# Optimization experiments

Hardware: AMD Instinct MI355X
Metric: run time of the kernel (lower is better)

The kernel has to match this reference:

```python
import math
import jax, jax.numpy as jnp
import numpy as np

B, T, D = 8, 2048, 256
N_TICKS, DT, P_MIN, P_MAX = 3, 1.0, 2.0, 4.0


def setup_inputs() -> dict:
    key = jax.random.key(0)
    ks = jax.random.split(key, 16)
    s = 1.0 / math.sqrt(D)
    w = lambda k: jax.random.normal(k, (D, D), jnp.float32) * s
    zb = jnp.zeros((D,), jnp.float32)
    return {
        "z": jax.random.normal(ks[0], (B, T, D), jnp.float32),
        "in_w": w(ks[1]), "in_b": zb,
        "ln_g": jnp.ones((D,), jnp.float32), "ln_b": zb,
        "q_w": w(ks[2]), "q_b": zb,
        "k_w": w(ks[3]), "k_b": zb,
        "v_w": w(ks[4]), "v_b": zb,
        "o_w": w(ks[5]), "o_b": zb,
        "log_tau": jnp.zeros((D,), jnp.float32),
        "p1_w": w(ks[6]), "p1_b": zb,
        "p2_w": w(ks[7]), "p2_b": zb,
    }


def _layernorm(x, g, b, eps=1e-5):
    mu = jnp.mean(x, axis=-1, keepdims=True)
    var = jnp.var(x, axis=-1, keepdims=True)
    return (x - mu) * jax.lax.rsqrt(var + eps) * g + b


def _lin(x, w, b):
    return x @ w.T + b


def reference(z, in_w, in_b, ln_g, ln_b, q_w, q_b, k_w, k_b, v_w, v_b,
              o_w, o_b, log_tau, p1_w, p1_b, p2_w, p2_b):
    tau = jnp.exp(log_tau)  # [d]
    inv_sqrt_d = 1.0 / math.sqrt(D)
    uniform = 1.0 / T
    pred_losses, eff_ps = [], []
    for _ in range(N_TICKS):
        h = _layernorm(_lin(z, in_w, in_b), ln_g, ln_b)
        Q, K, V = _lin(h, q_w, q_b), _lin(h, k_w, k_b), _lin(h, v_w, v_b)
        sim = jnp.einsum('btd,bsd->bts', Q, K) * inv_sqrt_d  # [B,T,T]
        attn = jax.nn.softmax(sim, axis=-1)
        row_max = jnp.max(attn, axis=-1)  # [B,T]
        conf = (jnp.mean(row_max, axis=-1) - uniform) / (1.0 - uniform + 1e-6)
        conf = jnp.clip(conf, 0.0, 1.0)  # [B]
        eff_p = P_MIN + (P_MAX - P_MIN) * conf
        eff_ps.append(jax.lax.stop_gradient(eff_p))
        attn_sharp = jax.nn.softmax(sim * eff_p[:, None, None], axis=-1)
        context = jnp.einsum('bts,bsd->btd', attn_sharp, V)
        target = _lin(context, o_w, o_b)
        z_pred = _lin(jax.nn.relu(_lin(z, p1_w, p1_b)), p2_w, p2_b)
        dz = (target - z) / (tau + 1e-6)
        z_next = z + DT * dz
        pred_losses.append(jnp.mean((z_pred - jax.lax.stop_gradient(z_next)) ** 2))
        z = z_next
    pred_loss_mean = jnp.mean(jnp.stack(pred_losses))
    eff_p_mean = jnp.mean(jnp.concatenate(eff_ps))
    return z, pred_loss_mean, eff_p_mean
```

## Files before the change

kernel.cpp:

```cpp
#include <hip/hip_runtime.h>
#include <math.h>

#define Bn 8
#define Tn 2048
#define Dn 256
#define NTICK 3
#define NROWS (Bn*Tn)
#define ABM 64
#define NBLKA (NROWS/ABM)
#define BS 64
#define GM 64
#define NBLKG (NROWS/GM)
#define WP 65536

typedef unsigned int u32;
typedef unsigned short u16;
typedef __attribute__((ext_vector_type(8))) short bf16x8;
typedef __attribute__((ext_vector_type(4))) float f32x4;

__device__ __forceinline__ float bf2f(u32 u){
  union { u32 i; float f; } x; x.i = u << 16; return x.f;
}
__device__ __forceinline__ u16 f2bf(float f){
  union { float f; u32 i; } x; x.f = f;
  u32 r = (x.i + 0x7fffu + ((x.i >> 16) & 1u)) >> 16;
  return (u16)r;
}
__device__ __forceinline__ void gld_lds16(const u16* gsrc, u16* ldst){
  __builtin_amdgcn_global_load_lds(
      (const __attribute__((address_space(1))) u32*)(const void*)gsrc,
      (__attribute__((address_space(3))) u32*)(void*)ldst, 16, 0, 0);
}

__device__ __forceinline__ void stage_A(const u16* __restrict__ A, int row0, char* smem){
  const int tid = threadIdx.x, lane = tid & 63, w = tid >> 6;
  #pragma unroll
  for (int r=0;r<8;++r){
    int s = w*16 + 2*r + (lane>>5);
    int slot = (lane & 31) ^ (s & 7);
    gld_lds16(A + (size_t)(row0 + s)*Dn + slot*8, (u16*)(smem + (w*16 + 2*r)*512));
  }
}
__device__ __forceinline__ void load_frags(const char* smem, bf16x8* af){
  const int tid = threadIdx.x, lane = tid & 63, w = tid >> 6;
  const int l7 = lane & 7, g = (lane >> 4) & 3, q15 = lane & 15;
  const char* ab = smem + (w*16 + q15)*512;
  #pragma unroll
  for (int kk=0;kk<8;++kk) af[kk] = *(const bf16x8*)(ab + 16*((4*kk+g)^l7));
}
__device__ __forceinline__ void stage_Wchunk(const u16* __restrict__ W, int c, char* wbuf){
  const int tid = threadIdx.x, lane = tid & 63, w = tid >> 6;
  #pragma unroll
  for (int r=0;r<2;++r){
    int rl = w*4 + 2*r + (lane>>5);
    int slot = (lane & 31) ^ (rl & 7);
    gld_lds16(W + (size_t)(c*16 + rl)*Dn + slot*8, (u16*)(wbuf + (w*4 + 2*r)*512));
  }
}
__device__ __forceinline__ void load_wfrags(const char* wbuf, bf16x8* wf){
  const int lane = threadIdx.x & 63;
  const int l7 = lane & 7, g = (lane >> 4) & 3, q15 = lane & 15;
  const char* wb_ = wbuf + q15*512;
  #pragma unroll
  for (int kk=0;kk<8;++kk) wf[kk] = *(const bf16x8*)(wb_ + 16*((4*kk+g)^l7));
}
__device__ __forceinline__ void zero_acc(f32x4* acc){
  #pragma unroll
  for (int nt=0;nt<16;++nt) acc[nt] = (f32x4){0.f,0.f,0.f,0.f};
}
#define CHUNK_STEP(c, NC, PLANE_OF, IDX_OF)                                    \
  asm volatile("s_waitcnt lgkmcnt(0)" ::: "memory");                           \
  if ((c) < (NC)-2) { asm volatile("s_waitcnt vmcnt(2)" ::: "memory"); }       \
  else              { asm volatile("s_waitcnt vmcnt(0)" ::: "memory"); }       \
  __builtin_amdgcn_sched_barrier(0);                                           \
  __builtin_amdgcn_s_barrier();                                                \
  if ((c)+3 < (NC)) stage_Wchunk(PLANE_OF((c)+3), IDX_OF((c)+3), ring + (((c)+3)&3)*8192);

__global__ void k_prep(const float* __restrict__ s0, const float* __restrict__ s1,
                       const float* __restrict__ s2, const float* __restrict__ s3,
                       const float* __restrict__ s4, const float* __restrict__ s5,
                       const float* __restrict__ s6, u16* __restrict__ dst){
  int y = blockIdx.y;
  const float* s = (y==0)?s0:(y==1)?s1:(y==2)?s2:(y==3)?s3:(y==4)?s4:(y==5)?s5:s6;
  int i = (blockIdx.x*256 + threadIdx.x)*4;
  float4 v = *(const float4*)(s + i);
  u16 h0=f2bf(v.x), h1=f2bf(v.y), h2=f2bf(v.z), h3=f2bf(v.w);
  uint2 hi, lo;
  hi.x = (u32)h0 | ((u32)h1 << 16);
  hi.y = (u32)h2 | ((u32)h3 << 16);
  lo.x = (u32)f2bf(v.x - bf2f(h0)) | ((u32)f2bf(v.y - bf2f(h1)) << 16);
  lo.y = (u32)f2bf(v.z - bf2f(h2)) | ((u32)f2bf(v.w - bf2f(h3)) << 16);
  *(uint2*)(dst + (size_t)y*WP + i) = hi;
  *(uint2*)(dst + (size_t)(7+y)*WP + i) = lo;
}

__global__ void k_split(const float* __restrict__ s, u16* __restrict__ dh, u16* __restrict__ dl,
                        float* __restrict__ stats){
  if (blockIdx.x == 0 && threadIdx.x < 64) stats[threadIdx.x] = 0.f;
  int i = (blockIdx.x*256 + threadIdx.x)*4;
  float4 v = *(const float4*)(s + i);
  u16 h0=f2bf(v.x), h1=f2bf(v.y), h2=f2bf(v.z), h3=f2bf(v.w);
  uint2 hi, lo;
  hi.x = (u32)h0 | ((u32)h1 << 16);
  hi.y = (u32)h2 | ((u32)h3 << 16);
  lo.x = (u32)f2bf(v.x - bf2f(h0)) | ((u32)f2bf(v.y - bf2f(h1)) << 16);
  lo.y = (u32)f2bf(v.z - bf2f(h2)) | ((u32)f2bf(v.w - bf2f(h3)) << 16);
  *(uint2*)(dh + i) = hi;
  *(uint2*)(dl + i) = lo;
}

__global__ __launch_bounds__(256) void k_gemm_ln(
    const u16* __restrict__ Ahi, const u16* __restrict__ Alo,
    const u16* __restrict__ Whi, const u16* __restrict__ Wlo,
    const float* __restrict__ bias, const float* __restrict__ gamma, const float* __restrict__ beta,
    u16* __restrict__ h)
{
  __shared__ __align__(16) char smem[65536];
  char* ring = smem;
  f32x4 acc[16];
  const int row0 = blockIdx.x * GM;
  stage_A(Ahi, row0, smem);
  stage_A(Alo, row0, smem + 32768);
  asm volatile("s_waitcnt vmcnt(0)" ::: "memory");
  __builtin_amdgcn_sched_barrier(0);
  bf16x8 afh[8], afl[8];
  load_frags(smem, afh);
  load_frags(smem + 32768, afl);
  asm volatile("s_waitcnt lgkmcnt(0)" ::: "memory");
  __builtin_amdgcn_sched_barrier(0);
  __builtin_amdgcn_s_barrier();
  zero_acc(acc);
  #define LN_PL(i) ((i) < 16 ? Whi : Wlo)
  #define LN_IX(i) ((i) & 15)
  stage_Wchunk(LN_PL(0), LN_IX(0), ring + 0*8192);
  stage_Wchunk(LN_PL(1), LN_IX(1), ring + 1*8192);
  stage_Wchunk(LN_PL(2), LN_IX(2), ring + 2*8192);
  asm volatile("s_waitcnt vmcnt(4)" ::: "memory");
  __builtin_amdgcn_sched_barrier(0);
  __builtin_amdgcn_s_barrier();
  for (int c=0; c<32; ++c){
    bf16x8 wf[8];
    load_wfrags(ring + (c&3)*8192, wf);
    int nt = c & 15;
    if (c < 16){
      #pragma unroll
      for (int kk=0;kk<8;++kk)
        acc[nt] = __builtin_amdgcn_mfma_f32_16x16x32_bf16(afh[kk], wf[kk], acc[nt], 0,0,0);
      #pragma unroll
      for (int kk=0;kk<8;++kk)
        acc[nt] = __builtin_amdgcn_mfma_f32_16x16x32_bf16(afl[kk], wf[kk], acc[nt], 0,0,0);
    } else {
      #pragma unroll
      for (int kk=0;kk<8;++kk)
        acc[nt] = __builtin_amdgcn_mfma_f32_16x16x32_bf16(afh[kk], wf[kk], acc[nt], 0,0,0);
    }
    CHUNK_STEP(c, 32, LN_PL, LN_IX)
  }
  const int tid = threadIdx.x, lane = tid & 63, w = tid >> 6;
  const int g4 = lane >> 4, q15 = lane & 15;
  float bcol[16], gcol[16], becol[16];
  #pragma unroll
  for (int nt=0;nt<16;++nt){
    int col = nt*16 + q15;
    bcol[nt] = bias[col]; gcol[nt] = gamma[col]; becol[nt] = beta[col];
  }
  float mu[4], rstd[4];
  #pragma unroll
  for (int j=0;j<4;++j){
    float s=0.f, q=0.f;
    #pragma unroll
    for (int nt=0;nt<16;++nt){ float v = acc[nt][j] + bcol[nt]; s += v; q += v*v; }
    #pragma unroll
    for (int off=1; off<16; off<<=1){ s += __shfl_xor(s,off); q += __shfl_xor(q,off); }
    float m = s*(1.f/Dn);
    mu[j] = m; rstd[j] = rsqrtf(q*(1.f/Dn) - m*m + 1e-5f);
  }
  const size_t rbase = (size_t)(row0 + w*16 + g4*4);
  #pragma unroll
  for (int nt=0;nt<16;++nt){
    #pragma unroll
    for (int j=0;j<4;++j){
      float v = (acc[nt][j] + bcol[nt] - mu[j])*rstd[j]*gcol[nt] + becol[nt];
      h[(rbase+j)*Dn + nt*16 + q15] = f2bf(v);
    }
  }
}

__global__ __launch_bounds__(256) void k_gemm_qkv(
    const u16* __restrict__ h, const u16* __restrict__ wbf,
    const float* __restrict__ qb, const float* __restrict__ kb, const float* __restrict__ vb,
    u16* __restrict__ Qo, u16* __restrict__ Ko, u16* __restrict__ Vo)
{
  const u16 *Whi, *Wlo; const float* bias; u16* out;
  if (blockIdx.y == 0){ Whi = wbf + 1*WP; Wlo = wbf + 8*WP;  bias = qb; out = Qo; }
  else if (blockIdx.y == 1){ Whi = wbf + 2*WP; Wlo = wbf + 9*WP;  bias = kb; out = Ko; }
  else { Whi = wbf + 3*WP; Wlo = wbf + 10*WP; bias = vb; out = Vo; }
  __shared__ __align__(16) char smem[65536];
  char* ring = smem + 32768;
  f32x4 acc[16];
  const int row0 = blockIdx.x * GM;
  stage_A(h, row0, smem);
  #define QK_PL(i) ((i) < 16 ? Whi : Wlo)
  #define QK_IX(i) ((i) & 15)
  stage_Wchunk(QK_PL(0), QK_IX(0), ring + 0*8192);
  stage_Wchunk(QK_PL(1), QK_IX(1), ring + 1*8192);
  stage_Wchunk(QK_PL(2), QK_IX(2), ring + 2*8192);
  asm volatile("s_waitcnt vmcnt(4)" ::: "memory");
  __builtin_amdgcn_sched_barrier(0);
  bf16x8 af[8];
  load_frags(smem, af);
  zero_acc(acc);
  __builtin_amdgcn_s_barrier();
  for (int c=0; c<32; ++c){
    bf16x8 wf[8];
    load_wfrags(ring + (c&3)*8192, wf);
    int nt = c & 15;
    #pragma unroll
    for (int kk=0;kk<8;++kk)
      acc[nt] = __builtin_amdgcn_mfma_f32_16x16x32_bf16(af[kk], wf[kk], acc[nt], 0,0,0);
    CHUNK_STEP(c, 32, QK_PL, QK_IX)
  }
  const int tid = threadIdx.x, lane = tid & 63, w = tid >> 6;
  const int g4 = lane >> 4, q15 = lane & 15;
  const size_t rbase = (size_t)(row0 + w*16 + g4*4);
  #pragma unroll
  for (int nt=0;nt<16;++nt){
    float bc = bias[nt*16 + q15];
    #pragma unroll
    for (int j=0;j<4;++j)
      out[(rbase+j)*Dn + nt*16 + q15] = f2bf(acc[nt][j] + bc);
  }
}

__global__ __launch_bounds__(256) void k_gemm_update(
    const u16* __restrict__ Chi, const u16* __restrict__ Clo,
    const u16* __restrict__ Whi, const u16* __restrict__ Wlo,
    const float* __restrict__ ob,
    const u16* __restrict__ zhi_old, const u16* __restrict__ zlo_old,
    const float* __restrict__ log_tau,
    u16* __restrict__ zhi_new, u16* __restrict__ zlo_new,
    float* __restrict__ zout)
{
  __shared__ __align__(16) char smem[65536];
  char* ring = smem;
  f32x4 acc[16];
  const int row0 = blockIdx.x * GM;
  stage_A(Chi, row0, smem);
  stage_A(Clo, row0, smem + 32768);
  asm volatile("s_waitcnt vmcnt(0)" ::: "memory");
  __builtin_amdgcn_sched_barrier(0);
  bf16x8 afh[8], afl[8];
  load_frags(smem, afh);
  load_frags(smem + 32768, afl);
  asm volatile("s_waitcnt lgkmcnt(0)" ::: "memory");
  __builtin_amdgcn_sched_barrier(0);
  __builtin_amdgcn_s_barrier();
  zero_acc(acc);
  stage_Wchunk(LN_PL(0), LN_IX(0), ring + 0*8192);
  stage_Wchunk(LN_PL(1), LN_IX(1), ring + 1*8192);
  stage_Wchunk(LN_PL(2), LN_IX(2), ring + 2*8192);
  asm volatile("s_waitcnt vmcnt(4)" ::: "memory");
  __builtin_amdgcn_sched_barrier(0);
  __builtin_amdgcn_s_barrier();
  for (int c=0; c<32; ++c){
    bf16x8 wf[8];
    load_wfrags(ring + (c&3)*8192, wf);
    int nt = c & 15;
    if (c < 16){
      #pragma unroll
      for (int kk=0;kk<8;++kk)
        acc[nt] = __builtin_amdgcn_mfma_f32_16x16x32_bf16(afh[kk], wf[kk], acc[nt], 0,0,0);
      #pragma unroll
      for (int kk=0;kk<8;++kk)
        acc[nt] = __builtin_amdgcn_mfma_f32_16x16x32_bf16(afl[kk], wf[kk], acc[nt], 0,0,0);
    } else {
      #pragma unroll
      for (int kk=0;kk<8;++kk)
        acc[nt] = __builtin_amdgcn_mfma_f32_16x16x32_bf16(afh[kk], wf[kk], acc[nt], 0,0,0);
    }
    CHUNK_STEP(c, 32, LN_PL, LN_IX)
  }
  const int tid = threadIdx.x, lane = tid & 63, w = tid >> 6;
  const int g4 = lane >> 4, q15 = lane & 15;
  const size_t rbase = (size_t)(row0 + w*16 + g4*4);
  #pragma unroll
  for (int nt=0;nt<16;++nt){
    int col = nt*16 + q15;
    float bc = ob[col];
    float invt = 1.f/(expf(log_tau[col]) + 1e-6f);
    #pragma unroll
    for (int j=0;j<4;++j){
      size_t idx = (rbase+j)*Dn + col;
      float zo = bf2f(zhi_old[idx]) + bf2f(zlo_old[idx]);
      float zn = zo + (acc[nt][j] + bc - zo)*invt;
      u16 zh = f2bf(zn);
      zhi_new[idx] = zh;
      zlo_new[idx] = f2bf(zn - bf2f(zh));
      if (zout) zout[idx] = zn;
    }
  }
}

__global__ __launch_bounds__(256) void k_gemm_relu(
    const u16* __restrict__ A, const u16* __restrict__ Wb, const float* __restrict__ bias,
    u16* __restrict__ t1)
{
  __shared__ __align__(16) char smem[65536];
  char* ring = smem + 32768;
  f32x4 acc[16];
  const int row0 = blockIdx.x * GM;
  stage_A(A, row0, smem);
  #define W1_PL(i) (Wb)
  #define W1_IX(i) (i)
  stage_Wchunk(Wb, 0, ring + 0*8192);
  stage_Wchunk(Wb, 1, ring + 1*8192);
  stage_Wchunk(Wb, 2, ring + 2*8192);
  asm volatile("s_waitcnt vmcnt(4)" ::: "memory");
  __builtin_amdgcn_sched_barrier(0);
  bf16x8 af[8];
  load_frags(smem, af);
  zero_acc(acc);
  __builtin_amdgcn_s_barrier();
  for (int c=0; c<16; ++c){
    bf16x8 wf[8];
    load_wfrags(ring + (c&3)*8192, wf);
    #pragma unroll
    for (int kk=0;kk<8;++kk)
      acc[c] = __builtin_amdgcn_mfma_f32_16x16x32_bf16(af[kk], wf[kk], acc[c], 0,0,0);
    CHUNK_STEP(c, 16, W1_PL, W1_IX)
  }
  const int tid = threadIdx.x, lane = tid & 63, w = tid >> 6;
  const int g4 = lane >> 4, q15 = lane & 15;
  const size_t rbase = (size_t)(row0 + w*16 + g4*4);
  #pragma unroll
  for (int nt=0;nt<16;++nt){
    float bc = bias[nt*16 + q15];
    #pragma unroll
    for (int j=0;j<4;++j)
      t1[(rbase+j)*Dn + nt*16 + q15] = f2bf(fmaxf(acc[nt][j] + bc, 0.f));
  }
}

__global__ __launch_bounds__(256) void k_gemm_loss(
    const u16* __restrict__ t1, const u16* __restrict__ Wb, const float* __restrict__ bias,
    const u16* __restrict__ zhi_new, const u16* __restrict__ zlo_new,
    float* __restrict__ loss_acc)
{
  __shared__ __align__(16) char smem[65536];
  __shared__ float red[4];
  char* ring = smem + 32768;
  f32x4 acc[16];
  const int row0 = blockIdx.x * GM;
  stage_A(t1, row0, smem);
  stage_Wchunk(Wb, 0, ring + 0*8192);
  stage_Wchunk(Wb, 1, ring + 1*8192);
  stage_Wchunk(Wb, 2, ring + 2*8192);
  asm volatile("s_waitcnt vmcnt(4)" ::: "memory");
  __builtin_amdgcn_sched_barrier(0);
  bf16x8 af[8];
  load_frags(smem, af);
  zero_acc(acc);
  __builtin_amdgcn_s_barrier();
  for (int c=0; c<16; ++c){
    bf16x8 wf[8];
    load_wfrags(ring + (c&3)*8192, wf);
    #pragma unroll
    for (int kk=0;kk<8;++kk)
      acc[c] = __builtin_amdgcn_mfma_f32_16x16x32_bf16(af[kk], wf[kk], acc[c], 0,0,0);
    CHUNK_STEP(c, 16, W1_PL, W1_IX)
  }
  const int tid = threadIdx.x, lane = tid & 63, w = tid >> 6;
  const int g4 = lane >> 4, q15 = lane & 15;
  const size_t rbase = (size_t)(row0 + w*16 + g4*4);
  float lsum = 0.f;
  #pragma unroll
  for (int nt=0;nt<16;++nt){
    float bc = bias[nt*16 + q15];
    #pragma unroll
    for (int j=0;j<4;++j){
      size_t idx = (rbase+j)*Dn + nt*16 + q15;
      float zn = bf2f(zhi_new[idx]) + bf2f(zlo_new[idx]);
      float dn = acc[nt][j] + bc - zn;
      lsum += dn*dn;
    }
  }
  #pragma unroll
  for (int off=1; off<64; off<<=1) lsum += __shfl_xor(lsum, off);
  if (lane == 0) red[w] = lsum;
  __syncthreads();
  if (tid == 0) atomicAdd(loss_acc, red[0]+red[1]+red[2]+red[3]);
}

__global__ __launch_bounds__(256) void k_passA(
    const u16* __restrict__ Qg, const u16* __restrict__ Kg,
    float* __restrict__ conf_b)
{
  __shared__ __align__(16) char smem[65536];
  const int tid = threadIdx.x;
  const int lane = tid & 63, w = tid >> 6;
  const int l7 = lane & 7, g = (lane >> 4) & 3, q15 = lane & 15;
  const int row0 = blockIdx.x * ABM;
  const int b = row0 >> 11;
  const size_t kbase = (size_t)b * Tn * Dn;

  #pragma unroll
  for (int r=0;r<8;++r){
    int s = w*16 + 2*r + (lane>>5);
    int slot = (lane & 31) ^ (s & 7);
    gld_lds16(Qg + (size_t)(row0 + s)*Dn + slot*8, (u16*)(smem + (w*16 + 2*r)*512));
  }
  asm volatile("s_waitcnt vmcnt(0)" ::: "memory");
  __builtin_amdgcn_sched_barrier(0);
  bf16x8 qf[8];
  {
    const char* qb = smem + (w*16 + q15)*512;
    #pragma unroll
    for (int kk=0;kk<8;++kk) qf[kk] = *(const bf16x8*)(qb + 16*((4*kk+g)^l7));
  }
  asm volatile("s_waitcnt lgkmcnt(0)" ::: "memory");
  __builtin_amdgcn_sched_barrier(0);
  #pragma unroll
  for (int r=0;r<8;++r){
    int s = w*16 + 2*r + (lane>>5);
    int slot = (lane & 31) ^ (s & 7);
    gld_lds16(Kg + kbase + (size_t)(s)*Dn + slot*8, (u16*)(smem + 32768 + (w*16 + 2*r)*512));
  }
  #pragma unroll
  for (int r=0;r<8;++r){
    int s = w*16 + 2*r + (lane>>5);
    int slot = (lane & 31) ^ (s & 7);
    gld_lds16(Kg + kbase + (size_t)(BS + s)*Dn + slot*8, (u16*)(smem + (w*16 + 2*r)*512));
  }
  asm volatile("s_waitcnt vmcnt(8)" ::: "memory");
  __builtin_amdgcn_sched_barrier(0);
  __builtin_amdgcn_s_barrier();

  float m_run = -INFINITY, l_run = 0.f;
  int cur = 1;
  for (int tile=0; tile<Tn/BS; ++tile){
    const char* kb = smem + cur*32768;
    f32x4 sc[4];
    #pragma unroll
    for (int ms=0;ms<4;++ms) sc[ms] = (f32x4){0.f,0.f,0.f,0.f};
    #pragma unroll
    for (int kk=0;kk<8;++kk){
      #pragma unroll
      for (int ms=0;ms<4;++ms){
        bf16x8 kf = *(const bf16x8*)(kb + (ms*16+q15)*512 + 16*((4*kk+g)^l7));
        sc[ms] = __builtin_amdgcn_mfma_f32_16x16x32_bf16(kf, qf[kk], sc[ms], 0,0,0);
      }
    }
    float vmax = -INFINITY;
    float vals[16];
    #pragma unroll
    for (int ms=0;ms<4;++ms){
      #pragma unroll
      for (int j=0;j<4;++j){ float v = sc[ms][j]*0.0625f; vals[ms*4+j]=v; vmax=fmaxf(vmax,v); }
    }
    vmax = fmaxf(vmax, __shfl_xor(vmax,16));
    vmax = fmaxf(vmax, __shfl_xor(vmax,32));
    float mnew = fmaxf(m_run, vmax);
    float corr = __expf(m_run - mnew);
    float esum = 0.f;
    #pragma unroll
    for (int t2=0;t2<16;++t2) esum += __expf(vals[t2]-mnew);
    esum += __shfl_xor(esum,16); esum += __shfl_xor(esum,32);
    l_run = l_run*corr + esum;
    m_run = mnew;

    asm volatile("s_waitcnt vmcnt(0)" ::: "memory");
    __builtin_amdgcn_sched_barrier(0);
    __builtin_amdgcn_s_barrier();
    if (tile < Tn/BS - 2){
      #pragma unroll
      for (int r=0;r<8;++r){
        int s = w*16 + 2*r + (lane>>5);
        int slot = (lane & 31) ^ (s & 7);
        gld_lds16(Kg + kbase + (size_t)((tile+2)*BS + s)*Dn + slot*8,
                  (u16*)(smem + cur*32768 + (w*16 + 2*r)*512));
      }
    }
    cur ^= 1;
  }
  float r1 = 1.f/l_run;
  #pragma unroll
  for (int off=1; off<64; off<<=1) r1 += __shfl_xor(r1, off);
  if (lane==0) atomicAdd(conf_b + b, r1*0.25f);
}

#define KB0 0
#define KB1 32768
#define VT0 65536
#define VT1 98304
#define PST 131072
__global__ __launch_bounds__(512) void k_passB(
    const u16* __restrict__ Qg, const u16* __restrict__ Kg, const u16* __restrict__ Vg,
    const float* __restrict__ conf_sum, u16* __restrict__ Chi, u16* __restrict__ Clo)
{
  __shared__ __align__(16) char smem[139264];
  const int tid = threadIdx.x;
  const int lane = tid & 63, w = tid >> 6;
  const int qg = w & 3, hs = w >> 2;
  const int l7 = lane & 7, g = (lane >> 4) & 3, q15 = lane & 15;
  const int row0 = blockIdx.x * ABM;
  const int b = row0 >> 11;
  const size_t kbase = (size_t)b * Tn * Dn;
  float mean_rm = conf_sum[b] * (1.f/Tn);
  float uniform = 1.f/Tn;
  float conf = fminf(fmaxf((mean_rm - uniform)/(1.f - uniform + 1e-6f), 0.f), 1.f);
  const float scale = (2.f + 2.f*conf) * 0.0625f;
  const int tid2 = tid & 255;
  const int dblk = tid2 >> 3, sblk = tid2 & 7;
  uint4 vreg[8];
  const int NT = Tn/BS;

  if (hs == 0){
    #pragma unroll
    for (int r=0;r<8;++r){
      int s = w*16 + 2*r + (lane>>5);
      int slot = (lane & 31) ^ (s & 7);
      gld_lds16(Qg + (size_t)(row0 + s)*Dn + slot*8, (u16*)(smem + KB0 + (w*16 + 2*r)*512));
    }
  } else {
    const u16* vsrc = Vg + kbase + (size_t)(sblk*8)*Dn + dblk*8;
    #pragma unroll
    for (int si=0; si<8; ++si) vreg[si] = *(const uint4*)(vsrc + (size_t)si*Dn);
  }
  __syncthreads();
  bf16x8 qf[8];
  {
    const char* qb = smem + KB0 + (qg*16 + q15)*512;
    #pragma unroll
    for (int kk=0;kk<8;++kk) qf[kk] = *(const bf16x8*)(qb + 16*((4*kk+g)^l7));
  }
  __syncthreads();
  if (hs == 0){
    #pragma unroll
    for (int r=0;r<8;++r){
      int s = w*16 + 2*r + (lane>>5);
      int slot = (lane & 31) ^ (s & 7);
      gld_lds16(Kg + kbase + (size_t)(s)*Dn + slot*8, (u16*)(smem + KB0 + (w*16 + 2*r)*512));
    }
    #pragma unroll
    for (int r=0;r<8;++r){
      int s = w*16 + 2*r + (lane>>5);
      int slot = (lane & 31) ^ (s & 7);
      gld_lds16(Kg + kbase + (size_t)(BS + s)*Dn + slot*8, (u16*)(smem + KB1 + (w*16 + 2*r)*512));
    }
    asm volatile("s_waitcnt vmcnt(8)" ::: "memory");
    __builtin_amdgcn_sched_barrier(0);
  } else {
    const u32* rw = (const u32*)vreg;
    #pragma unroll
    for (int dl=0; dl<8; ++dl){
      int wi = dl >> 1;
      u32 sel = (dl & 1) ? 0x07060302u : 0x05040100u;
      uint4 o;
      o.x = __builtin_amdgcn_perm(rw[1*4+wi], rw[0*4+wi], sel);
      o.y = __builtin_amdgcn_perm(rw[3*4+wi], rw[2*4+wi], sel);
      o.z = __builtin_amdgcn_perm(rw[5*4+wi], rw[4*4+wi], sel);
      o.w = __builtin_amdgcn_perm(rw[7*4+wi], rw[6*4+wi], sel);
      int d = dblk*8 + dl;
      *(uint4*)(smem + VT0 + d*128 + 16*(sblk ^ dl)) = o;
    }
    asm volatile("s_waitcnt lgkmcnt(0)" ::: "memory");
    __builtin_amdgcn_sched_barrier(0);
  }
  __builtin_amdgcn_s_barrier();

  float m_run = -INFINITY, l_run = 0.f;
  f32x4 oa[16];
  #pragma unroll
  for (int md=0;md<16;++md) oa[md] = (f32x4){0.f,0.f,0.f,0.f};

  char* pbase = smem + PST + w*1024 + q15*64;
  const int psw = q15 & 3;

  int cur = 0;
  for (int tile=0; tile<NT; ++tile){
    const char* kbuf = smem + (cur ? KB1 : KB0);
    const char* vbuf = smem + (cur ? VT1 : VT0);
    char* vbuf_n = (char*)smem + (cur ? VT0 : VT1);
    if (hs == 1 && tile < NT-1){
      const u16* vsrc = Vg + kbase + (size_t)((tile+1)*BS + sblk*8)*Dn + dblk*8;
      #pragma unroll
      for (int si=0; si<8; ++si) vreg[si] = *(const uint4*)(vsrc + (size_t)si*Dn);
    }
    f32x4 sc[2];
    sc[0] = (f32x4){0.f,0.f,0.f,0.f};
    sc[1] = (f32x4){0.f,0.f,0.f,0.f};
    #pragma unroll
    for (int kk=0;kk<8;++kk){
      #pragma unroll
      for (int msl=0;msl<2;++msl){
        int msg = 2*hs + msl;
        bf16x8 kf = *(const bf16x8*)(kbuf + (msg*16+q15)*512 + 16*((4*kk+g)^l7));
        sc[msl] = __builtin_amdgcn_mfma_f32_16x16x32_bf16(kf, qf[kk], sc[msl], 0,0,0);
      }
    }
    float vmax = -INFINITY;
    float vals[8];
    #pragma unroll
    for (int msl=0;msl<2;++msl){
      #pragma unroll
      for (int j=0;j<4;++j){ float v = sc[msl][j]*scale; vals[msl*4+j]=v; vmax=fmaxf(vmax,v); }
    }
    vmax = fmaxf(vmax, __shfl_xor(vmax,16));
    vmax = fmaxf(vmax, __shfl_xor(vmax,32));
    float mnew = fmaxf(m_run, vmax);
    float corr = __expf(m_run - mnew);
    float esum = 0.f;
    #pragma unroll
    for (int t2=0;t2<8;++t2){ float p = __expf(vals[t2]-mnew); vals[t2]=p; esum += p; }
    esum += __shfl_xor(esum,16); esum += __shfl_xor(esum,32);
    l_run = l_run*corr + esum;
    m_run = mnew;
    #pragma unroll
    for (int md=0;md<16;++md) oa[md] *= corr;
    #pragma unroll
    for (int msl=0;msl<2;++msl){
      uint2 pw;
      pw.x = (u32)f2bf(vals[msl*4+0]) | ((u32)f2bf(vals[msl*4+1]) << 16);
      pw.y = (u32)f2bf(vals[msl*4+2]) | ((u32)f2bf(vals[msl*4+3]) << 16);
      int slot = (2*msl + (g>>1)) ^ psw;
      *(uint2*)(pbase + slot*16 + (g&1)*8) = pw;
    }
    asm volatile("s_waitcnt lgkmcnt(0)" ::: "memory");
    __builtin_amdgcn_sched_barrier(0);
    {
      bf16x8 pf = *(const bf16x8*)(pbase + ((g ^ psw)*16));
      #pragma unroll
      for (int md=0; md<16; ++md){
        bf16x8 vf = *(const bf16x8*)(vbuf + (md*16+q15)*128 + 16*((4*hs+g)^l7));
        oa[md] = __builtin_amdgcn_mfma_f32_16x16x32_bf16(vf, pf, oa[md], 0,0,0);
      }
    }
    if (hs == 1){
      if (tile < NT-1){
        asm volatile("s_waitcnt vmcnt(0)" ::: "memory");
        __builtin_amdgcn_sched_barrier(0);
        const u32* rw = (const u32*)vreg;
        #pragma unroll
        for (int dl=0; dl<8; ++dl){
          int wi = dl >> 1;
          u32 sel = (dl & 1) ? 0x07060302u : 0x05040100u;
          uint4 o;
          o.x = __builtin_amdgcn_perm(rw[1*4+wi], rw[0*4+wi], sel);
          o.y = __builtin_amdgcn_perm(rw[3*4+wi], rw[2*4+wi], sel);
          o.z = __builtin_amdgcn_perm(rw[5*4+wi], rw[4*4+wi], sel);
          o.w = __builtin_amdgcn_perm(rw[7*4+wi], rw[6*4+wi], sel);
          int d = dblk*8 + dl;
          *(uint4*)(vbuf_n + d*128 + 16*(sblk ^ dl)) = o;
        }
      }
      asm volatile("s_waitcnt lgkmcnt(0)" ::: "memory");
    } else {
      asm volatile("s_waitcnt vmcnt(0) lgkmcnt(0)" ::: "memory");
    }
    __builtin_amdgcn_sched_barrier(0);
    __builtin_amdgcn_s_barrier();
    if (hs == 0 && tile < NT-2){
      #pragma unroll
      for (int r=0;r<8;++r){
        int s = w*16 + 2*r + (lane>>5);
        int slot = (lane & 31) ^ (s & 7);
        gld_lds16(Kg + kbase + (size_t)((tile+2)*BS + s)*Dn + slot*8,
                  (u16*)(smem + (cur ? KB1 : KB0) + (w*16 + 2*r)*512));
      }
    }
    cur ^= 1;
  }
  __syncthreads();
  if (hs == 1){
    char* ob_ = smem + (qg*64 + lane)*256;
    #pragma unroll
    for (int md=0; md<16; ++md)
      *(f32x4*)(ob_ + (md ^ q15)*16) = oa[md];
    float2 ml; ml.x = m_run; ml.y = l_run;
    *(float2*)(smem + VT0 + (qg*64 + lane)*8) = ml;
  }
  __syncthreads();
  if (hs == 0){
    float2 ml = *(const float2*)(smem + VT0 + (qg*64 + lane)*8);
    float m = fmaxf(m_run, ml.x);
    float ca = __expf(m_run - m), cb = __expf(ml.x - m);
    float l = l_run*ca + ml.y*cb;
    float inv = 1.f / l;
    const char* ob_ = smem + (qg*64 + lane)*256;
    const size_t rr = (size_t)(row0 + qg*16 + q15)*Dn + g*4;
    #pragma unroll
    for (int md=0; md<16; ++md){
      f32x4 ob = *(const f32x4*)(ob_ + (md ^ q15)*16);
      float v0 = (oa[md][0]*ca + ob[0]*cb)*inv;
      float v1 = (oa[md][1]*ca + ob[1]*cb)*inv;
      float v2 = (oa[md][2]*ca + ob[2]*cb)*inv;
      float v3 = (oa[md][3]*ca + ob[3]*cb)*inv;
      uint2 hi, lo;
      u16 h0=f2bf(v0), h1=f2bf(v1), h2=f2bf(v2), h3=f2bf(v3);
      hi.x = (u32)h0 | ((u32)h1 << 16);
      hi.y = (u32)h2 | ((u32)h3 << 16);
      lo.x = (u32)f2bf(v0 - bf2f(h0)) | ((u32)f2bf(v1 - bf2f(h1)) << 16);
      lo.y = (u32)f2bf(v2 - bf2f(h2)) | ((u32)f2bf(v3 - bf2f(h3)) << 16);
      *(uint2*)(Chi + rr + md*16) = hi;
      *(uint2*)(Clo + rr + md*16) = lo;
    }
  }
}

__global__ void k_finalize(const float* __restrict__ loss3, const float* __restrict__ conf_sum,
                           float* __restrict__ out_scalars){
  if (threadIdx.x == 0){
    float ls = (loss3[0]+loss3[1]+loss3[2]) * (1.f/(3.f*NROWS*Dn));
    float es = 0.f;
    float uniform = 1.f/Tn;
    #pragma unroll
    for (int i=0;i<NTICK*Bn;++i){
      float mean_rm = conf_sum[i] * (1.f/Tn);
      float conf = fminf(fmaxf((mean_rm - uniform)/(1.f - uniform + 1e-6f), 0.f), 1.f);
      es += 2.f + 2.f*conf;
    }
    out_scalars[0] = ls;
    out_scalars[1] = es * (1.f/(NTICK*Bn));
  }
}

extern "C" void kernel_launch(void* const* d_in, const int* in_sizes, int n_in,
                              void* d_out, int out_size, void* d_ws, size_t ws_size,
                              hipStream_t stream) {
  (void)in_sizes; (void)n_in; (void)out_size; (void)ws_size;
  const float* z_in   = (const float*)d_in[0];
  const float* in_w   = (const float*)d_in[1];
  const float* in_b   = (const float*)d_in[2];
  const float* ln_g   = (const float*)d_in[3];
  const float* ln_b   = (const float*)d_in[4];
  const float* q_w    = (const float*)d_in[5];
  const float* q_b    = (const float*)d_in[6];
  const float* k_w    = (const float*)d_in[7];
  const float* k_b    = (const float*)d_in[8];
  const float* v_w    = (const float*)d_in[9];
  const float* v_b    = (const float*)d_in[10];
  const float* o_w    = (const float*)d_in[11];
  const float* o_b    = (const float*)d_in[12];
  const float* log_tau= (const float*)d_in[13];
  const float* p1_w   = (const float*)d_in[14];
  const float* p1_b   = (const float*)d_in[15];
  const float* p2_w   = (const float*)d_in[16];
  const float* p2_b   = (const float*)d_in[17];

  float* out = (float*)d_out;
  const size_t NE = (size_t)NROWS * Dn;

  u16*  zh0  = (u16*)d_ws;
  u16*  zl0  = zh0 + NE;
  u16*  zh1  = zl0 + NE;
  u16*  zl1  = zh1 + NE;
  u16*  hbuf = zl1 + NE;
  u16*  Qb   = hbuf + NE;
  u16*  Kb   = Qb + NE;
  u16*  Vb   = Kb + NE;
  u16*  Chi  = Vb + NE;
  u16*  Clo  = Chi + NE;
  u16*  t1b  = Clo + NE;
  u16*  wbf  = t1b + NE;
  float* stats = (float*)(wbf + 14*WP);
  float* conf_sum = stats;
  float* loss     = stats + 24;

  k_prep<<<dim3(64,7), 256, 0, stream>>>(in_w, q_w, k_w, v_w, o_w, p1_w, p2_w, wbf);
  k_split<<<4096, 256, 0, stream>>>(z_in, zh0, zl0, stats);

  u16* zh_list[2] = { zh0, zh1 };
  u16* zl_list[2] = { zl0, zl1 };

  for (int t = 0; t < NTICK; ++t){
    u16* zh_old = zh_list[t & 1];
    u16* zl_old = zl_list[t & 1];
    u16* zh_new = zh_list[(t+1) & 1];
    u16* zl_new = zl_list[(t+1) & 1];
    float* zout = (t == NTICK-1) ? out : nullptr;
    k_gemm_ln<<<NBLKG, 256, 0, stream>>>(zh_old, zl_old, wbf + 0*WP, wbf + 7*WP,
                                         in_b, ln_g, ln_b, hbuf);
    k_gemm_qkv<<<dim3(NBLKG,3), 256, 0, stream>>>(hbuf, wbf, q_b, k_b, v_b, Qb, Kb, Vb);
    k_passA<<<NBLKA, 256, 0, stream>>>(Qb, Kb, conf_sum + t*8);
    k_passB<<<NBLKA, 512, 0, stream>>>(Qb, Kb, Vb, conf_sum + t*8, Chi, Clo);
    k_gemm_update<<<NBLKG, 256, 0, stream>>>(Chi, Clo, wbf + 4*WP, wbf + 11*WP, o_b,
                                             zh_old, zl_old, log_tau, zh_new, zl_new, zout);
    k_gemm_relu<<<NBLKG, 256, 0, stream>>>(zh_old, wbf + 5*WP, p1_b, t1b);
    k_gemm_loss<<<NBLKG, 256, 0, stream>>>(t1b, wbf + 6*WP, p2_b, zh_new, zl_new, loss + t);
  }
  k_finalize<<<1, 64, 0, stream>>>(loss, conf_sum, out + NE);
}
```

Before: 802.7 us.

## Fuse QKV projections per block and use 32x32 MFMA in passA

The QKV kernel now has each block loop over all three weight matrices (96 chunks) while reusing its staged A tile, instead of launching three blocks per row tile. Each projection's output is written and the accumulators reset every 32 chunks. In passA, the score computation switches from 16x16x32 to 32x32x16 MFMA, with waves split into query and key halves, and the two halves' partial softmax statistics are merged through LDS. This aims to cut redundant A loads and LDS fragment traffic, but it reduces QKV grid parallelism by 3x and adds a merge step in passA.

```diff
diff --git a/kernel.cpp b/kernel.cpp
--- a/kernel.cpp
+++ b/kernel.cpp
@@ -17,6 +17,7 @@
 typedef unsigned short u16;
 typedef __attribute__((ext_vector_type(8))) short bf16x8;
 typedef __attribute__((ext_vector_type(4))) float f32x4;
+typedef __attribute__((ext_vector_type(16))) float f32x16;
 
 __device__ __forceinline__ float bf2f(u32 u){
   union { u32 i; float f; } x; x.i = u << 16; return x.f;
@@ -191,44 +192,46 @@
     const float* __restrict__ qb, const float* __restrict__ kb, const float* __restrict__ vb,
     u16* __restrict__ Qo, u16* __restrict__ Ko, u16* __restrict__ Vo)
 {
-  const u16 *Whi, *Wlo; const float* bias; u16* out;
-  if (blockIdx.y == 0){ Whi = wbf + 1*WP; Wlo = wbf + 8*WP;  bias = qb; out = Qo; }
-  else if (blockIdx.y == 1){ Whi = wbf + 2*WP; Wlo = wbf + 9*WP;  bias = kb; out = Ko; }
-  else { Whi = wbf + 3*WP; Wlo = wbf + 10*WP; bias = vb; out = Vo; }
   __shared__ __align__(16) char smem[65536];
   char* ring = smem + 32768;
   f32x4 acc[16];
   const int row0 = blockIdx.x * GM;
   stage_A(h, row0, smem);
-  #define QK_PL(i) ((i) < 16 ? Whi : Wlo)
-  #define QK_IX(i) ((i) & 15)
-  stage_Wchunk(QK_PL(0), QK_IX(0), ring + 0*8192);
-  stage_Wchunk(QK_PL(1), QK_IX(1), ring + 1*8192);
-  stage_Wchunk(QK_PL(2), QK_IX(2), ring + 2*8192);
+  #define QKV_PL(i) (wbf + ((size_t)((((i)>>5)+1) + (((i)>>4)&1)*7))*WP)
+  #define QKV_IX(i) ((i) & 15)
+  stage_Wchunk(QKV_PL(0), QKV_IX(0), ring + 0*8192);
+  stage_Wchunk(QKV_PL(1), QKV_IX(1), ring + 1*8192);
+  stage_Wchunk(QKV_PL(2), QKV_IX(2), ring + 2*8192);
   asm volatile("s_waitcnt vmcnt(4)" ::: "memory");
   __builtin_amdgcn_sched_barrier(0);
   bf16x8 af[8];
   load_frags(smem, af);
   zero_acc(acc);
-  __builtin_amdgcn_s_barrier();
-  for (int c=0; c<32; ++c){
+  const int tid = threadIdx.x, lane = tid & 63, w = tid >> 6;
+  const int g4 = lane >> 4, q15 = lane & 15;
+  const size_t rbase = (size_t)(row0 + w*16 + g4*4);
+  __builtin_amdgcn_s_barrier();
+  for (int c=0; c<96; ++c){
     bf16x8 wf[8];
     load_wfrags(ring + (c&3)*8192, wf);
     int nt = c & 15;
     #pragma unroll
     for (int kk=0;kk<8;++kk)
       acc[nt] = __builtin_amdgcn_mfma_f32_16x16x32_bf16(af[kk], wf[kk], acc[nt], 0,0,0);
-    CHUNK_STEP(c, 32, QK_PL, QK_IX)
-  }
-  const int tid = threadIdx.x, lane = tid & 63, w = tid >> 6;
-  const int g4 = lane >> 4, q15 = lane & 15;
-  const size_t rbase = (size_t)(row0 + w*16 + g4*4);
-  #pragma unroll
-  for (int nt=0;nt<16;++nt){
-    float bc = bias[nt*16 + q15];
-    #pragma unroll
-    for (int j=0;j<4;++j)
-      out[(rbase+j)*Dn + nt*16 + q15] = f2bf(acc[nt][j] + bc);
+    CHUNK_STEP(c, 96, QKV_PL, QKV_IX)
+    if ((c & 31) == 31){
+      int p = c >> 5;
+      const float* bias = (p==0) ? qb : (p==1) ? kb : vb;
+      u16* out = (p==0) ? Qo : (p==1) ? Ko : Vo;
+      #pragma unroll
+      for (int nt2=0;nt2<16;++nt2){
+        float bc = bias[nt2*16 + q15];
+        #pragma unroll
+        for (int j=0;j<4;++j)
+          out[(rbase+j)*Dn + nt2*16 + q15] = f2bf(acc[nt2][j] + bc);
+      }
+      zero_acc(acc);
+    }
   }
 }
 
@@ -398,7 +401,8 @@
   __shared__ __align__(16) char smem[65536];
   const int tid = threadIdx.x;
   const int lane = tid & 63, w = tid >> 6;
-  const int l7 = lane & 7, g = (lane >> 4) & 3, q15 = lane & 15;
+  const int l31 = lane & 31, hi5 = lane >> 5;
+  const int qh = w >> 1, sh = w & 1;
   const int row0 = blockIdx.x * ABM;
   const int b = row0 >> 11;
   const size_t kbase = (size_t)b * Tn * Dn;
@@ -411,14 +415,17 @@
   }
   asm volatile("s_waitcnt vmcnt(0)" ::: "memory");
   __builtin_amdgcn_sched_barrier(0);
-  bf16x8 qf[8];
+  __builtin_amdgcn_s_barrier();
+  bf16x8 qf[16];
   {
-    const char* qb = smem + (w*16 + q15)*512;
-    #pragma unroll
-    for (int kk=0;kk<8;++kk) qf[kk] = *(const bf16x8*)(qb + 16*((4*kk+g)^l7));
+    const char* qb = smem + (qh*32 + l31)*512;
+    const int r7 = l31 & 7;
+    #pragma unroll
+    for (int t=0;t<16;++t) qf[t] = *(const bf16x8*)(qb + 16*((2*t+hi5)^r7));
   }
   asm volatile("s_waitcnt lgkmcnt(0)" ::: "memory");
   __builtin_amdgcn_sched_barrier(0);
+  __builtin_amdgcn_s_barrier();
   #pragma unroll
   for (int r=0;r<8;++r){
     int s = w*16 + 2*r + (lane>>5);
@@ -436,35 +443,27 @@
   __builtin_amdgcn_s_barrier();
 
   float m_run = -INFINITY, l_run = 0.f;
+  const int sr7 = l31 & 7;
   int cur = 1;
   for (int tile=0; tile<Tn/BS; ++tile){
-    const char* kb = smem + cur*32768;
-    f32x4 sc[4];
-    #pragma unroll
-    for (int ms=0;ms<4;++ms) sc[ms] = (f32x4){0.f,0.f,0.f,0.f};
-    #pragma unroll
-    for (int kk=0;kk<8;++kk){
-      #pragma unroll
-      for (int ms=0;ms<4;++ms){
-        bf16x8 kf = *(const bf16x8*)(kb + (ms*16+q15)*512 + 16*((4*kk+g)^l7));
-        sc[ms] = __builtin_amdgcn_mfma_f32_16x16x32_bf16(kf, qf[kk], sc[ms], 0,0,0);
-      }
+    const char* kb = smem + cur*32768 + (sh*32 + l31)*512;
+    f32x16 sc = (f32x16)(0.f);
+    #pragma unroll
+    for (int t=0;t<16;++t){
+      bf16x8 kf = *(const bf16x8*)(kb + 16*((2*t+hi5)^sr7));
+      sc = __builtin_amdgcn_mfma_f32_32x32x16_bf16(kf, qf[t], sc, 0,0,0);
     }
     float vmax = -INFINITY;
     float vals[16];
     #pragma unroll
-    for (int ms=0;ms<4;++ms){
-      #pragma unroll
-      for (int j=0;j<4;++j){ float v = sc[ms][j]*0.0625f; vals[ms*4+j]=v; vmax=fmaxf(vmax,v); }
-    }
-    vmax = fmaxf(vmax, __shfl_xor(vmax,16));
+    for (int i=0;i<16;++i){ float v = sc[i]*0.0625f; vals[i]=v; vmax=fmaxf(vmax,v); }
     vmax = fmaxf(vmax, __shfl_xor(vmax,32));
     float mnew = fmaxf(m_run, vmax);
     float corr = __expf(m_run - mnew);
     float esum = 0.f;
     #pragma unroll
-    for (int t2=0;t2<16;++t2) esum += __expf(vals[t2]-mnew);
-    esum += __shfl_xor(esum,16); esum += __shfl_xor(esum,32);
+    for (int i=0;i<16;++i) esum += __expf(vals[i]-mnew);
+    esum += __shfl_xor(esum,32);
     l_run = l_run*corr + esum;
     m_run = mnew;
 
@@ -482,10 +481,21 @@
     }
     cur ^= 1;
   }
-  float r1 = 1.f/l_run;
-  #pragma unroll
-  for (int off=1; off<64; off<<=1) r1 += __shfl_xor(r1, off);
-  if (lane==0) atomicAdd(conf_b + b, r1*0.25f);
+  __syncthreads();
+  if (sh == 1 && lane < 32){
+    float2 ml; ml.x = m_run; ml.y = l_run;
+    *(float2*)(smem + (qh*32 + l31)*8) = ml;
+  }
+  __syncthreads();
+  if (sh == 0){
+    float2 o = *(const float2*)(smem + (qh*32 + l31)*8);
+    float m2 = fmaxf(m_run, o.x);
+    float lm = l_run*__expf(m_run - m2) + o.y*__expf(o.x - m2);
+    float r1 = 1.f/lm;
+    #pragma unroll
+    for (int off=1; off<64; off<<=1) r1 += __shfl_xor(r1, off);
+    if (lane==0) atomicAdd(conf_b + b, r1*0.5f);
+  }
 }
 
 #define KB0 0
@@ -780,7 +790,7 @@
     float* zout = (t == NTICK-1) ? out : nullptr;
     k_gemm_ln<<<NBLKG, 256, 0, stream>>>(zh_old, zl_old, wbf + 0*WP, wbf + 7*WP,
                                          in_b, ln_g, ln_b, hbuf);
-    k_gemm_qkv<<<dim3(NBLKG,3), 256, 0, stream>>>(hbuf, wbf, q_b, k_b, v_b, Qb, Kb, Vb);
+    k_gemm_qkv<<<NBLKG, 256, 0, stream>>>(hbuf, wbf, q_b, k_b, v_b, Qb, Kb, Vb);
     k_passA<<<NBLKA, 256, 0, stream>>>(Qb, Kb, conf_sum + t*8);
     k_passB<<<NBLKA, 512, 0, stream>>>(Qb, Kb, Vb, conf_sum + t*8, Chi, Clo);
     k_gemm_update<<<NBLKG, 256, 0, stream>>>(Chi, Clo, wbf + 4*WP, wbf + 11*WP, o_b,
```

Result: slower. 893.7 us (+11.3%).
